# Kernel tuning notes

Hardware: AMD Instinct MI355X
Metric: run time of the kernel (lower is better)

The kernel has to match this reference:

```python
import jax, jax.numpy as jnp
import numpy as np

LN_EPS = 1e-5

def _layer_norm(x, g, b):
    m = x.mean(axis=-1, keepdims=True)
    v = x.var(axis=-1, keepdims=True)
    return (x - m) * jax.lax.rsqrt(v + LN_EPS) * g + b

def setup_inputs() -> dict:
    key = jax.random.key(0)
    ks = jax.random.split(key, 8)
    B, T, Din, D = 4, 4096, 1024, 1024
    s = 0.02
    return {
        "x": jax.random.normal(ks[0], (B, T, Din), jnp.float32),
        "hidden": jnp.zeros((B, 1, D), jnp.float32),
        "rnn_start": jnp.zeros((B, T, 1), jnp.float32),
        # EnsembleLinear(input_dim, d_model, ensemble=2): [2, Din, D] weights
        "Win": jax.random.normal(ks[1], (2, Din, D), jnp.float32) * s,
        "bin_": jnp.zeros((2, D), jnp.float32),
        "Wout": jax.random.normal(ks[2], (D, D), jnp.float32) * s,
        "bout": jnp.zeros((D,), jnp.float32),
        "W1": jax.random.normal(ks[3], (D, D), jnp.float32) * s,
        "b1": jnp.zeros((D,), jnp.float32),
        "W2": jax.random.normal(ks[4], (D, D), jnp.float32) * s,
        "b2": jnp.zeros((D,), jnp.float32),
        "ln_g": jnp.ones((D,), jnp.float32),
        "ln_b": jnp.zeros((D,), jnp.float32),
    }

def reference(x, hidden, rnn_start, Win, bin_, Wout, bout, W1, b1, W2, b2, ln_g, ln_b):
    # in_proj (ensemble of 2 linears): u[0]=v, u[1]=f
    u = jnp.einsum('btd,edk->ebtk', x, Win) + bin_[:, None, None, :]
    v = jnp.tanh(u[0])                      # [B,T,D]
    f = jax.nn.sigmoid(u[1])                # [B,T,D]
    f = f * (1.0 - rnn_start)               # reset gate at episode starts
    # gated linear recurrence (tied input gate): h_t = f_t*h_{t-1} + (1-f_t)*v_t
    h0 = hidden[:, 0, :]                    # [B,D]
    def step(h, vf):
        vt, ft = vf
        h = ft * h + (1.0 - ft) * vt
        return h, h
    hT, hs = jax.lax.scan(step, h0, (jnp.swapaxes(v, 0, 1), jnp.swapaxes(f, 0, 1)))
    hs = jnp.swapaxes(hs, 0, 1)             # [B,T,D]
    out = hs @ Wout + bout
    # PositionWiseFeedForward (dropout=0, eval): LN(w2(gelu(w1(x))) + x)
    x_ = jax.nn.gelu(out @ W1 + b1, approximate=False)
    out = _layer_norm(x_ @ W2 + b2 + out, ln_g, ln_b)
    hidden_new = hT[None, :, :]             # [1,B,D] (transpose(0,1) of [B,1,D])
    return out, hidden_new
```

## Files before the change

### kernel.cpp

```cpp
#include <hip/hip_runtime.h>
#include <hip/hip_bf16.h>
#include <math.h>

typedef __hip_bfloat16 bf16;
typedef __bf16  bf16x8  __attribute__((ext_vector_type(8)));
typedef float   floatx4 __attribute__((ext_vector_type(4)));

typedef const __attribute__((address_space(1))) void global_cv_t;
typedef __attribute__((address_space(3))) void       lds_v_t;

static __device__ __forceinline__ float bf2f(bf16 h) { return __bfloat162float(h); }
static __device__ __forceinline__ bf16  f2bf(float f) { return __float2bfloat16(f); }

__device__ __forceinline__ void load_lds16(const void* g, void* l) {
    __builtin_amdgcn_global_load_lds((global_cv_t*)g, (lds_v_t*)l, 16, 0, 0);
}

__global__ __launch_bounds__(256) void convx_k(const float4* __restrict__ in,
                                               bf16* __restrict__ out)
{
    const int i = blockIdx.x * 256 + threadIdx.x;
    const float4 v = in[i];
    bf16* o = out + (size_t)i * 4;
    o[0] = f2bf(v.x); o[1] = f2bf(v.y); o[2] = f2bf(v.z); o[3] = f2bf(v.w);
}

__global__ __launch_bounds__(256) void trc_k(
    const float* __restrict__ w0, const float* __restrict__ w1,
    const float* __restrict__ w2, const float* __restrict__ w3,
    const float* __restrict__ w4, bf16* __restrict__ dst)
{
    const float* src;
    switch (blockIdx.z) {
        case 0: src = w0; break;
        case 1: src = w1; break;
        case 2: src = w2; break;
        case 3: src = w3; break;
        default: src = w4; break;
    }
    bf16* d = dst + ((size_t)blockIdx.z << 20);
    __shared__ float tile[32][33];
    const int tx = threadIdx.x & 31;
    const int ty = threadIdx.x >> 5;
    const int bx = blockIdx.x * 32, by = blockIdx.y * 32;
#pragma unroll
    for (int j = 0; j < 32; j += 8)
        tile[ty + j][tx] = src[(size_t)(by + ty + j) * 1024 + bx + tx];
    __syncthreads();
#pragma unroll
    for (int j = 0; j < 32; j += 8)
        d[(size_t)(bx + ty + j) * 1024 + by + tx] = f2bf(tile[tx][ty + j]);
}

__global__ __launch_bounds__(256, 2) void gemmdb_k(
    const bf16* __restrict__ A, const bf16* __restrict__ Bt,
    const float* __restrict__ bias, const float* __restrict__ auxf,
    const bf16* __restrict__ auxb, bf16* __restrict__ Db,
    bf16* __restrict__ Db2, float* __restrict__ Df, const int mode)
{
    __shared__ alignas(16) bf16 As[2][128 * 64];
    __shared__ alignas(16) bf16 Bs[2][128 * 64];

    const int tid  = threadIdx.x;
    const int wave = tid >> 6;
    const int lane = tid & 63;
    const int quad = lane >> 4;
    const int l16  = lane & 15;
    const int sw   = l16 & 7;
    const int wm   = wave & 1;
    const int wn   = wave >> 1;
    const int bm   = blockIdx.x * 128;

    int bn, emode;
    const bf16* Bte = Bt;
    const float* biase = bias;
    bf16* Dbe = Db;
    if (mode == 5) {
        const int mat = blockIdx.y >> 3;
        bn    = (blockIdx.y & 7) * 128;
        Bte   = Bt + ((size_t)mat << 20);
        biase = bias + (mat << 10);
        Dbe   = mat ? Db2 : Db;
        emode = mat ? 1 : 0;
    } else {
        bn = blockIdx.y * 128;
        emode = mode;
    }

    const int srow  = lane >> 3;
    const int skoff = (((lane & 7) ^ srow) << 3);

    const bf16* gA = A   + (size_t)(bm + wave * 32 + srow) * 1024 + skoff;
    const bf16* gB = Bte + (size_t)(bn + wave * 32 + srow) * 1024 + skoff;

#define STAGE(BUF, KT) do {                                                       \
        _Pragma("unroll")                                                         \
        for (int c_ = 0; c_ < 4; ++c_) {                                          \
            load_lds16(gA + (size_t)c_ * 8192 + (KT) * 64,                        \
                       &As[BUF][wave * 2048 + c_ * 512]);                         \
            load_lds16(gB + (size_t)c_ * 8192 + (KT) * 64,                        \
                       &Bs[BUF][wave * 2048 + c_ * 512]);                         \
        }                                                                         \
    } while (0)

    floatx4 acc[4][4];
#pragma unroll
    for (int i = 0; i < 4; ++i)
#pragma unroll
        for (int j = 0; j < 4; ++j)
            acc[i][j] = (floatx4){0.f, 0.f, 0.f, 0.f};

#define COMPUTE(BUF) do {                                                         \
        _Pragma("unroll")                                                         \
        for (int kk_ = 0; kk_ < 2; ++kk_) {                                       \
            bf16x8 af_[4], bf_[4];                                                \
            _Pragma("unroll")                                                     \
            for (int t_ = 0; t_ < 4; ++t_) {                                      \
                const int g_ = ((kk_ * 4 + quad) ^ sw) << 3;                      \
                af_[t_] = *(const bf16x8*)&As[BUF][                               \
                    (wm * 64 + t_ * 16 + l16) * 64 + g_];                         \
                bf_[t_] = *(const bf16x8*)&Bs[BUF][                               \
                    (wn * 64 + t_ * 16 + l16) * 64 + g_];                         \
            }                                                                     \
            _Pragma("unroll")                                                     \
            for (int tm_ = 0; tm_ < 4; ++tm_)                                     \
                _Pragma("unroll")                                                 \
                for (int tn_ = 0; tn_ < 4; ++tn_)                                 \
                    acc[tm_][tn_] = __builtin_amdgcn_mfma_f32_16x16x32_bf16(      \
                        af_[tm_], bf_[tn_], acc[tm_][tn_], 0, 0, 0);              \
        }                                                                         \
    } while (0)

    STAGE(0, 0);
    __syncthreads();

#pragma unroll 1
    for (int it = 0; it < 8; ++it) {
        STAGE(1, 2 * it + 1);
        COMPUTE(0);
        __syncthreads();
        if (it < 7) STAGE(0, 2 * it + 2);
        COMPUTE(1);
        __syncthreads();
    }

#undef STAGE
#undef COMPUTE

    float bv[4];
#pragma unroll
    for (int tn = 0; tn < 4; ++tn)
        bv[tn] = biase[bn + wn * 64 + tn * 16 + l16];

#pragma unroll
    for (int tm = 0; tm < 4; ++tm) {
#pragma unroll
        for (int r = 0; r < 4; ++r) {
            const int gm = bm + wm * 64 + tm * 16 + quad * 4 + r;
            const size_t rowoff = (size_t)gm << 10;
            float rowmul = 1.f;
            if (emode == 1) rowmul = 1.f - auxf[gm];
#pragma unroll
            for (int tn = 0; tn < 4; ++tn) {
                const int gn = bn + wn * 64 + tn * 16 + l16;
                float val = acc[tm][tn][r] + bv[tn];
                if (emode == 0)      val = tanhf(val);
                else if (emode == 1) val = rowmul / (1.f + expf(-val));
                else if (emode == 3) val = 0.5f * val * (1.f + erff(val * 0.70710678118654752f));
                if (emode == 4) {
                    val += bf2f(auxb[rowoff + gn]);
                    Df[rowoff + gn] = val;
                } else {
                    Dbe[rowoff + gn] = f2bf(val);
                }
            }
        }
    }
}

__global__ __launch_bounds__(256) void scan1_k(
    const bf16* __restrict__ v, const bf16* __restrict__ f,
    float* __restrict__ Ac, float* __restrict__ Bc)
{
    const int idx = blockIdx.x * 256 + threadIdx.x;
    const int ch = idx & 4095;
    const int c  = idx >> 12;
    const int b  = ch >> 10, d = ch & 1023;
    const size_t base = ((size_t)(b * 4096 + c * 64) << 10) + d;
    float a = 1.f, hb = 0.f;
#pragma unroll 8
    for (int i = 0; i < 64; ++i) {
        const size_t o = base + ((size_t)i << 10);
        const float ft = bf2f(f[o]);
        const float vt = bf2f(v[o]);
        hb = fmaf(ft, hb, (1.f - ft) * vt);
        a *= ft;
    }
    Ac[c * 4096 + ch] = a;
    Bc[c * 4096 + ch] = hb;
}

__global__ __launch_bounds__(256) void scanmid_k(
    const float* __restrict__ Ac, const float* __restrict__ Bc,
    const float* __restrict__ hidden, float* __restrict__ Hin)
{
    const int ch = blockIdx.x * 256 + threadIdx.x;
    float h = hidden[ch];
#pragma unroll 8
    for (int c = 0; c < 64; ++c) {
        Hin[c * 4096 + ch] = h;
        h = fmaf(Ac[c * 4096 + ch], h, Bc[c * 4096 + ch]);
    }
}

__global__ __launch_bounds__(256) void scan2_k(
    const bf16* __restrict__ v, const bf16* __restrict__ f,
    const float* __restrict__ Hin, bf16* __restrict__ hs,
    float* __restrict__ hT)
{
    const int idx = blockIdx.x * 256 + threadIdx.x;
    const int ch = idx & 4095;
    const int c  = idx >> 12;
    const int b  = ch >> 10, d = ch & 1023;
    const size_t base = ((size_t)(b * 4096 + c * 64) << 10) + d;
    float h = Hin[c * 4096 + ch];
#pragma unroll 8
    for (int i = 0; i < 64; ++i) {
        const size_t o = base + ((size_t)i << 10);
        const float ft = bf2f(f[o]);
        const float vt = bf2f(v[o]);
        h = fmaf(ft, h, (1.f - ft) * vt);
        hs[o] = f2bf(h);
    }
    if (c == 63) hT[ch] = h;
}

__global__ __launch_bounds__(256) void ln_k(
    float* __restrict__ s, const float* __restrict__ g,
    const float* __restrict__ b)
{
    const int row = blockIdx.x;
    const int tid = threadIdx.x;
    const size_t off = (size_t)row << 10;
    const float4 xv = ((const float4*)(s + off))[tid];
    float sum = xv.x + xv.y + xv.z + xv.w;
    float sq  = xv.x * xv.x + xv.y * xv.y + xv.z * xv.z + xv.w * xv.w;
#pragma unroll
    for (int o = 32; o > 0; o >>= 1) {
        sum += __shfl_down(sum, o, 64);
        sq  += __shfl_down(sq,  o, 64);
    }
    __shared__ float s1[4], s2[4];
    if ((tid & 63) == 0) { s1[tid >> 6] = sum; s2[tid >> 6] = sq; }
    __syncthreads();
    sum = s1[0] + s1[1] + s1[2] + s1[3];
    sq  = s2[0] + s2[1] + s2[2] + s2[3];
    const float mean = sum * (1.f / 1024.f);
    const float var  = sq * (1.f / 1024.f) - mean * mean;
    const float rstd = rsqrtf(var + 1e-5f);
    const float4 gv = ((const float4*)g)[tid];
    const float4 bv = ((const float4*)b)[tid];
    float4 y;
    y.x = (xv.x - mean) * rstd * gv.x + bv.x;
    y.y = (xv.y - mean) * rstd * gv.y + bv.y;
    y.z = (xv.z - mean) * rstd * gv.z + bv.z;
    y.w = (xv.w - mean) * rstd * gv.w + bv.w;
    ((float4*)(s + off))[tid] = y;
}

extern "C" void kernel_launch(void* const* d_in, const int* in_sizes, int n_in,
                              void* d_out, int out_size, void* d_ws, size_t ws_size,
                              hipStream_t stream)
{
    const float* x         = (const float*)d_in[0];
    const float* hidden    = (const float*)d_in[1];
    const float* rnn_start = (const float*)d_in[2];
    const float* Win       = (const float*)d_in[3];
    const float* bin_      = (const float*)d_in[4];
    const float* Wout      = (const float*)d_in[5];
    const float* bout      = (const float*)d_in[6];
    const float* W1        = (const float*)d_in[7];
    const float* b1        = (const float*)d_in[8];
    const float* W2        = (const float*)d_in[9];
    const float* b2        = (const float*)d_in[10];
    const float* ln_g      = (const float*)d_in[11];
    const float* ln_b      = (const float*)d_in[12];
    float* out = (float*)d_out;
    float* hT  = out + (1u << 24);

    char* p = (char*)d_ws;
    bf16* Wt    = (bf16*)p;                    p += 5ull * (1u << 20) * sizeof(bf16);
    bf16* slotA = (bf16*)p;                    p += (1ull << 24) * sizeof(bf16);
    bf16* slotB = (bf16*)p;                    p += (1ull << 24) * sizeof(bf16);
    bf16* slotC = (bf16*)p;                    p += (1ull << 24) * sizeof(bf16);
    float* Ac  = (float*)p;                    p += (1ull << 18) * sizeof(float);
    float* Bc  = (float*)p;                    p += (1ull << 18) * sizeof(float);
    float* Hin = (float*)p;                    p += (1ull << 18) * sizeof(float);

    bf16* WoutT = Wt + 2u * (1u << 20);
    bf16* W1T   = Wt + 3u * (1u << 20);
    bf16* W2T   = Wt + 4u * (1u << 20);

    convx_k<<<16384, 256, 0, stream>>>((const float4*)x, slotA);
    trc_k<<<dim3(32, 32, 5), 256, 0, stream>>>(Win, Win + (1u << 20), Wout, W1, W2, Wt);

    gemmdb_k<<<dim3(128, 16), 256, 0, stream>>>(slotA, Wt, bin_, rnn_start, nullptr,
                                                slotB, slotC, nullptr, 5);

    scan1_k<<<1024, 256, 0, stream>>>(slotB, slotC, Ac, Bc);
    scanmid_k<<<16, 256, 0, stream>>>(Ac, Bc, hidden, Hin);
    scan2_k<<<1024, 256, 0, stream>>>(slotB, slotC, Hin, slotA, hT);

    gemmdb_k<<<dim3(128, 8), 256, 0, stream>>>(slotA, WoutT, bout, nullptr, nullptr,
                                               slotB, nullptr, nullptr, 2);
    gemmdb_k<<<dim3(128, 8), 256, 0, stream>>>(slotB, W1T,   b1,   nullptr, nullptr,
                                               slotC, nullptr, nullptr, 3);
    gemmdb_k<<<dim3(128, 8), 256, 0, stream>>>(slotC, W2T,   b2,   nullptr, slotB,
                                               nullptr, nullptr, out, 4);

    ln_k<<<16384, 256, 0, stream>>>(out, ln_g, ln_b);
}
```

Baseline: 479.7 us.

## Single-buffer GEMM LDS for higher occupancy, remap blocks by XCD, fast tanh/sigmoid

The GEMM kernel drops LDS double buffering in favour of a single 32 KB tile per block and raises launch bounds to 4 blocks per CU, so occupancy rather than explicit prefetch is meant to hide load latency. It also permutes the linear block id so that consecutive blocks on the same XCD share A-row tiles, aiming for better L2 reuse. The epilogue replaces tanhf and expf with __expf-based formulas. The cost is that loads and MFMA are no longer overlapped within a block, a possible register-pressure squeeze under the tighter launch bound, and slightly lower transcendental accuracy.

```diff
diff --git a/kernel.cpp b/kernel.cpp
--- a/kernel.cpp
+++ b/kernel.cpp
@@ -52,14 +52,14 @@
         d[(size_t)(bx + ty + j) * 1024 + by + tx] = f2bf(tile[tx][ty + j]);
 }
 
-__global__ __launch_bounds__(256, 2) void gemmdb_k(
+__global__ __launch_bounds__(256, 4) void gemm_k(
     const bf16* __restrict__ A, const bf16* __restrict__ Bt,
     const float* __restrict__ bias, const float* __restrict__ auxf,
     const bf16* __restrict__ auxb, bf16* __restrict__ Db,
     bf16* __restrict__ Db2, float* __restrict__ Df, const int mode)
 {
-    __shared__ alignas(16) bf16 As[2][128 * 64];
-    __shared__ alignas(16) bf16 Bs[2][128 * 64];
+    __shared__ alignas(16) bf16 As[128 * 64];
+    __shared__ alignas(16) bf16 Bs[128 * 64];
 
     const int tid  = threadIdx.x;
     const int wave = tid >> 6;
@@ -69,21 +69,29 @@
     const int sw   = l16 & 7;
     const int wm   = wave & 1;
     const int wn   = wave >> 1;
-    const int bm   = blockIdx.x * 128;
+
+    const int NBY  = gridDim.y;
+    const int nwg  = gridDim.x * NBY;
+    int bid = blockIdx.y * gridDim.x + blockIdx.x;
+    bid = (bid & 7) * (nwg >> 3) + (bid >> 3);
+    const int nysh = (NBY == 16) ? 4 : 3;
+    const int mi   = bid >> nysh;
+    const int ny   = bid & (NBY - 1);
+    const int bm   = mi * 128;
 
     int bn, emode;
     const bf16* Bte = Bt;
     const float* biase = bias;
     bf16* Dbe = Db;
     if (mode == 5) {
-        const int mat = blockIdx.y >> 3;
-        bn    = (blockIdx.y & 7) * 128;
+        const int mat = ny >> 3;
+        bn    = (ny & 7) * 128;
         Bte   = Bt + ((size_t)mat << 20);
         biase = bias + (mat << 10);
         Dbe   = mat ? Db2 : Db;
         emode = mat ? 1 : 0;
     } else {
-        bn = blockIdx.y * 128;
+        bn = ny * 128;
         emode = mode;
     }
 
@@ -92,16 +100,8 @@
 
     const bf16* gA = A   + (size_t)(bm + wave * 32 + srow) * 1024 + skoff;
     const bf16* gB = Bte + (size_t)(bn + wave * 32 + srow) * 1024 + skoff;
-
-#define STAGE(BUF, KT) do {                                                       \
-        _Pragma("unroll")                                                         \
-        for (int c_ = 0; c_ < 4; ++c_) {                                          \
-            load_lds16(gA + (size_t)c_ * 8192 + (KT) * 64,                        \
-                       &As[BUF][wave * 2048 + c_ * 512]);                         \
-            load_lds16(gB + (size_t)c_ * 8192 + (KT) * 64,                        \
-                       &Bs[BUF][wave * 2048 + c_ * 512]);                         \
-        }                                                                         \
-    } while (0)
+    bf16* lA = &As[wave * 2048];
+    bf16* lB = &Bs[wave * 2048];
 
     floatx4 acc[4][4];
 #pragma unroll
@@ -110,42 +110,32 @@
         for (int j = 0; j < 4; ++j)
             acc[i][j] = (floatx4){0.f, 0.f, 0.f, 0.f};
 
-#define COMPUTE(BUF) do {                                                         \
-        _Pragma("unroll")                                                         \
-        for (int kk_ = 0; kk_ < 2; ++kk_) {                                       \
-            bf16x8 af_[4], bf_[4];                                                \
-            _Pragma("unroll")                                                     \
-            for (int t_ = 0; t_ < 4; ++t_) {                                      \
-                const int g_ = ((kk_ * 4 + quad) ^ sw) << 3;                      \
-                af_[t_] = *(const bf16x8*)&As[BUF][                               \
-                    (wm * 64 + t_ * 16 + l16) * 64 + g_];                         \
-                bf_[t_] = *(const bf16x8*)&Bs[BUF][                               \
-                    (wn * 64 + t_ * 16 + l16) * 64 + g_];                         \
-            }                                                                     \
-            _Pragma("unroll")                                                     \
-            for (int tm_ = 0; tm_ < 4; ++tm_)                                     \
-                _Pragma("unroll")                                                 \
-                for (int tn_ = 0; tn_ < 4; ++tn_)                                 \
-                    acc[tm_][tn_] = __builtin_amdgcn_mfma_f32_16x16x32_bf16(      \
-                        af_[tm_], bf_[tn_], acc[tm_][tn_], 0, 0, 0);              \
-        }                                                                         \
-    } while (0)
-
-    STAGE(0, 0);
-    __syncthreads();
-
-#pragma unroll 1
-    for (int it = 0; it < 8; ++it) {
-        STAGE(1, 2 * it + 1);
-        COMPUTE(0);
+    for (int k0 = 0; k0 < 1024; k0 += 64) {
         __syncthreads();
-        if (it < 7) STAGE(0, 2 * it + 2);
-        COMPUTE(1);
+#pragma unroll
+        for (int c = 0; c < 4; ++c) {
+            load_lds16(gA + (size_t)c * 8192 + k0, lA + c * 512);
+            load_lds16(gB + (size_t)c * 8192 + k0, lB + c * 512);
+        }
         __syncthreads();
-    }
-
-#undef STAGE
-#undef COMPUTE
+
+#pragma unroll
+        for (int kk = 0; kk < 2; ++kk) {
+            bf16x8 af[4], bfr[4];
+#pragma unroll
+            for (int t = 0; t < 4; ++t) {
+                const int g = ((kk * 4 + quad) ^ sw) << 3;
+                af[t]  = *(const bf16x8*)&As[(wm * 64 + t * 16 + l16) * 64 + g];
+                bfr[t] = *(const bf16x8*)&Bs[(wn * 64 + t * 16 + l16) * 64 + g];
+            }
+#pragma unroll
+            for (int tm = 0; tm < 4; ++tm)
+#pragma unroll
+                for (int tn = 0; tn < 4; ++tn)
+                    acc[tm][tn] = __builtin_amdgcn_mfma_f32_16x16x32_bf16(
+                        af[tm], bfr[tn], acc[tm][tn], 0, 0, 0);
+        }
+    }
 
     float bv[4];
 #pragma unroll
@@ -164,8 +154,8 @@
             for (int tn = 0; tn < 4; ++tn) {
                 const int gn = bn + wn * 64 + tn * 16 + l16;
                 float val = acc[tm][tn][r] + bv[tn];
-                if (emode == 0)      val = tanhf(val);
-                else if (emode == 1) val = rowmul / (1.f + expf(-val));
+                if (emode == 0)      val = 1.f - 2.f / (1.f + __expf(2.f * val));
+                else if (emode == 1) val = rowmul / (1.f + __expf(-val));
                 else if (emode == 3) val = 0.5f * val * (1.f + erff(val * 0.70710678118654752f));
                 if (emode == 4) {
                     val += bf2f(auxb[rowoff + gn]);
@@ -304,19 +294,19 @@
     convx_k<<<16384, 256, 0, stream>>>((const float4*)x, slotA);
     trc_k<<<dim3(32, 32, 5), 256, 0, stream>>>(Win, Win + (1u << 20), Wout, W1, W2, Wt);
 
-    gemmdb_k<<<dim3(128, 16), 256, 0, stream>>>(slotA, Wt, bin_, rnn_start, nullptr,
-                                                slotB, slotC, nullptr, 5);
+    gemm_k<<<dim3(128, 16), 256, 0, stream>>>(slotA, Wt, bin_, rnn_start, nullptr,
+                                              slotB, slotC, nullptr, 5);
 
     scan1_k<<<1024, 256, 0, stream>>>(slotB, slotC, Ac, Bc);
     scanmid_k<<<16, 256, 0, stream>>>(Ac, Bc, hidden, Hin);
     scan2_k<<<1024, 256, 0, stream>>>(slotB, slotC, Hin, slotA, hT);
 
-    gemmdb_k<<<dim3(128, 8), 256, 0, stream>>>(slotA, WoutT, bout, nullptr, nullptr,
-                                               slotB, nullptr, nullptr, 2);
-    gemmdb_k<<<dim3(128, 8), 256, 0, stream>>>(slotB, W1T,   b1,   nullptr, nullptr,
-                                               slotC, nullptr, nullptr, 3);
-    gemmdb_k<<<dim3(128, 8), 256, 0, stream>>>(slotC, W2T,   b2,   nullptr, slotB,
-                                               nullptr, nullptr, out, 4);
+    gemm_k<<<dim3(128, 8), 256, 0, stream>>>(slotA, WoutT, bout, nullptr, nullptr,
+                                             slotB, nullptr, nullptr, 2);
+    gemm_k<<<dim3(128, 8), 256, 0, stream>>>(slotB, W1T,   b1,   nullptr, nullptr,
+                                             slotC, nullptr, nullptr, 3);
+    gemm_k<<<dim3(128, 8), 256, 0, stream>>>(slotC, W2T,   b2,   nullptr, slotB,
+                                             nullptr, nullptr, out, 4);
 
     ln_k<<<16384, 256, 0, stream>>>(out, ln_g, ln_b);
 }
```

After: 423.9 us. -11.6%, faster.
